# Kernel optimization log

Measured on AMD Instinct MI355X. Metric: run time of the kernel, lower is better.

## Reference

```python
import jax, jax.numpy as jnp
import numpy as np
from jax import lax

B, D, C, K = 8192, 512, 1000, 8
EPS = 1e-8
TEMP = 0.2
NEG = -10000.0


def setup_inputs() -> dict:
    key = jax.random.key(0)
    ks = jax.random.split(key, 6)
    z = jax.random.normal(ks[0], (B, D), dtype=jnp.float32)
    n_exp = jax.random.randint(ks[1], (B,), 0, K, dtype=jnp.int32)
    s1 = 1.0 / np.sqrt(D)
    W1 = jax.random.normal(ks[2], (K, D, D), dtype=jnp.float32) * s1
    b1 = jax.random.normal(ks[3], (K, D), dtype=jnp.float32) * 0.01
    W2 = jax.random.normal(ks[4], (K, D, C), dtype=jnp.float32) * s1
    b2 = jax.random.normal(ks[5], (K, C), dtype=jnp.float32) * 0.01
    return {"z": z, "n_exp": n_exp, "W1": W1, "b1": b1, "W2": W2, "b2": b2}


def _gates_one(p, c, n):
    # p: [K,C] softmax probs for one sample; c: [K] confidences; n: scalar int
    pn = p / (jnp.linalg.norm(p, axis=-1, keepdims=True) + EPS)
    S = pn @ pn.T  # [K,K] pairwise cosine similarity
    sel0 = jnp.zeros((K,), dtype=bool).at[jnp.argmax(c)].set(True)

    def body(t, sel):
        # max cosine sim of each candidate to already-selected set
        max_sim = jnp.max(jnp.where(sel[None, :], S, -jnp.inf), axis=1)
        dist = jnp.where(sel, -jnp.inf, 1.0 - max_sim)
        new = sel.at[jnp.argmax(dist)].set(True)
        return jnp.where(t < n, new, sel)

    sel = lax.fori_loop(1, K, body, sel0)
    gate_logits = jnp.where(sel, c, NEG) / TEMP
    return jax.nn.softmax(gate_logits)


def reference(z, n_exp, W1, b1, W2, b2):
    # K expert MLPs, batched: [B,d] -> [B,K,C]
    h = jax.nn.relu(jnp.einsum('bd,kde->bke', z, W1) + b1[None])
    logits_all = jnp.einsum('bke,kec->bkc', h, W2) + b2[None]
    probs = jax.nn.softmax(logits_all, axis=-1)
    conf = jnp.max(probs, axis=-1)  # [B,K]
    gates = jax.vmap(_gates_one)(probs, conf, n_exp)  # [B,K]
    logits = jnp.einsum('bkc,bk->bc', logits_all, gates)
    return logits, gates
```

## Files before the change

kernel.cpp:

```cpp
#include <hip/hip_runtime.h>
#include <math.h>

#define B_SZ 8192
#define D_DIM 512
#define C_DIM 1000
#define C_PAD 1024
#define K_EXP 8
#define TEMP_INV 5.0f
#define EPS_N 1e-8f

typedef __attribute__((ext_vector_type(8))) short frag_ab;
typedef __attribute__((ext_vector_type(4))) float frag_cd;

__device__ __forceinline__ short f2bf(float f) {
    unsigned u = __builtin_bit_cast(unsigned, f);
    unsigned r = (u + 0x7fffu + ((u >> 16) & 1u)) >> 16;
    return (short)r;
}
__device__ __forceinline__ float bf2f(short s) {
    unsigned u = ((unsigned)(unsigned short)s) << 16;
    return __builtin_bit_cast(float, u);
}
__device__ __forceinline__ void split2(float v, short& s0, short& s1) {
    s0 = f2bf(v);
    s1 = f2bf(v - bf2f(s0));
}

__device__ __forceinline__ void gl_lds16(const short* g, short* l) {
    __builtin_amdgcn_global_load_lds(
        (const __attribute__((address_space(1))) unsigned int*)(const void*)g,
        (__attribute__((address_space(3))) unsigned int*)(void*)l,
        16, 0, 0);
}

__global__ __launch_bounds__(256) void prep_z(const float* __restrict__ z,
                                              short* __restrict__ p0, short* __restrict__ p1) {
    int idx = blockIdx.x * 256 + threadIdx.x;
    float v = z[idx];
    short a, b; split2(v, a, b);
    p0[idx] = a; p1[idx] = b;
}

__global__ __launch_bounds__(256) void prep_w1t(const float* __restrict__ W1,
                                                short* __restrict__ p0, short* __restrict__ p1) {
    __shared__ float t[32][33];
    const int k = blockIdx.z;
    const int d0 = blockIdx.x * 32;
    const int e0 = blockIdx.y * 32;
    const int tx = threadIdx.x & 31, ty = threadIdx.x >> 5;
    const float* src = W1 + ((size_t)k << 18);
#pragma unroll
    for (int r = 0; r < 4; r++) {
        int d = d0 + ty + 8 * r;
        t[ty + 8 * r][tx] = src[(size_t)d * 512 + e0 + tx];
    }
    __syncthreads();
#pragma unroll
    for (int r = 0; r < 4; r++) {
        int e = e0 + ty + 8 * r;
        int d = d0 + tx;
        float v = t[tx][ty + 8 * r];
        short a, b; split2(v, a, b);
        size_t o = ((size_t)k << 18) + (size_t)e * 512 + d;
        p0[o] = a; p1[o] = b;
    }
}

__global__ __launch_bounds__(256) void prep_w2t(const float* __restrict__ W2,
                                                short* __restrict__ p0, short* __restrict__ p1) {
    __shared__ float t[32][33];
    const int k = blockIdx.z;
    const int e0 = blockIdx.x * 32;
    const int c0 = blockIdx.y * 32;
    const int tx = threadIdx.x & 31, ty = threadIdx.x >> 5;
    const float* src = W2 + (size_t)k * (D_DIM * C_DIM);
#pragma unroll
    for (int r = 0; r < 4; r++) {
        int e = e0 + ty + 8 * r;
        int c = c0 + tx;
        t[ty + 8 * r][tx] = (c < C_DIM) ? src[(size_t)e * C_DIM + c] : 0.f;
    }
    __syncthreads();
#pragma unroll
    for (int r = 0; r < 4; r++) {
        int c = c0 + ty + 8 * r;
        int e = e0 + tx;
        float v = t[tx][ty + 8 * r];
        short a, b; split2(v, a, b);
        size_t o = (size_t)k * (C_PAD * D_DIM) + (size_t)c * 512 + e;
        p0[o] = a; p1[o] = b;
    }
}

__global__ __launch_bounds__(256, 2) void gemm_split(
    const short* __restrict__ A0, const short* __restrict__ A1, long long aBatch,
    const short* __restrict__ B0, const short* __restrict__ B1, long long bBatch,
    const float* __restrict__ bias, int biasBatch,
    float* __restrict__ Cf, long long cBatch, int ldc, int Nout,
    short* __restrict__ H0, short* __restrict__ H1, long long hBatch,
    int mt, int nt, int mode)
{
    const int lin = blockIdx.x;
    const int k = lin & 7;
    const int rem = lin >> 3;
    const int gm = (mt >= 4) ? 4 : mt;
    const int win = rem / (gm * nt);
    const int local = rem % (gm * nt);
    const int m0 = (win * gm + local / nt) * 128;
    const int n0 = (local % nt) * 128;

    const int tid = threadIdx.x;
    const int lane = tid & 63;
    const int wv = tid >> 6;
    const int wm = (wv & 1) * 64;
    const int wn = (wv >> 1) * 64;

    __shared__ short lds[32768];

    const short* gA0 = A0 + (size_t)k * aBatch + (size_t)m0 * 512;
    const short* gA1 = A1 + (size_t)k * aBatch + (size_t)m0 * 512;
    const short* gB0 = B0 + (size_t)k * bBatch + (size_t)n0 * 512;
    const short* gB1 = B1 + (size_t)k * bBatch + (size_t)n0 * 512;

    frag_cd acc[4][4];
#pragma unroll
    for (int i = 0; i < 4; i++)
#pragma unroll
        for (int j = 0; j < 4; j++)
            acc[i][j] = (frag_cd){0.f, 0.f, 0.f, 0.f};

    const int srow = tid >> 2;
    const int sch  = (tid & 3) * 8;

    auto stage = [&](int k0, short* buf) {
        short* bA = buf;
        short* bB = buf + 8192;
        const short* ga[2] = {gA0, gA1};
        const short* gb[2] = {gB0, gB1};
#pragma unroll
        for (int p = 0; p < 2; p++)
#pragma unroll
            for (int hh = 0; hh < 2; hh++) {
                int row = hh * 64 + srow;
                gl_lds16(ga[p] + (size_t)row * 512 + k0 + sch, bA + p * 4096 + row * 32 + sch);
                gl_lds16(gb[p] + (size_t)row * 512 + k0 + sch, bB + p * 4096 + row * 32 + sch);
            }
    };

    stage(0, lds);

    for (int it = 0; it < 16; it++) {
        short* curb = lds + (it & 1) * 16384;
        short* nxtb = lds + ((it + 1) & 1) * 16384;
        __syncthreads();
        if (it + 1 < 16) stage((it + 1) * 32, nxtb);

        short* ldsA = curb;
        short* ldsB = curb + 8192;
        frag_ab af[2][4], bfr[2][4];
#pragma unroll
        for (int p = 0; p < 2; p++)
#pragma unroll
            for (int t = 0; t < 4; t++) {
                af[p][t]  = *(const frag_ab*)(ldsA + p * 4096 + (wm + t * 16 + (lane & 15)) * 32 + (lane >> 4) * 8);
                bfr[p][t] = *(const frag_ab*)(ldsB + p * 4096 + (wn + t * 16 + (lane & 15)) * 32 + (lane >> 4) * 8);
            }

#pragma unroll
        for (int i = 0; i < 4; i++)
#pragma unroll
            for (int j = 0; j < 4; j++) {
                frag_cd c = acc[i][j];
                c = __builtin_amdgcn_mfma_f32_16x16x32_bf16(af[0][i], bfr[0][j], c, 0, 0, 0);
                c = __builtin_amdgcn_mfma_f32_16x16x32_bf16(af[0][i], bfr[1][j], c, 0, 0, 0);
                c = __builtin_amdgcn_mfma_f32_16x16x32_bf16(af[1][i], bfr[0][j], c, 0, 0, 0);
                acc[i][j] = c;
            }
    }

    const int r0 = (lane >> 4) * 4;
    const int cc = lane & 15;
    if (mode == 0) {
        float* C = Cf + (size_t)k * cBatch;
        const float* bb = bias + (size_t)k * biasBatch;
#pragma unroll
        for (int i = 0; i < 4; i++) {
            int rowb = m0 + wm + i * 16 + r0;
#pragma unroll
            for (int j = 0; j < 4; j++) {
                int col = n0 + wn + j * 16 + cc;
                if (col < Nout) {
                    float b = bb[col];
#pragma unroll
                    for (int r = 0; r < 4; r++)
                        C[(size_t)(rowb + r) * ldc + col] = acc[i][j][r] + b;
                }
            }
        }
    } else {
        short* h0 = H0 + (size_t)k * hBatch;
        short* h1 = H1 + (size_t)k * hBatch;
        const float* bb = bias + (size_t)k * biasBatch;
#pragma unroll
        for (int i = 0; i < 4; i++) {
            int rowb = m0 + wm + i * 16 + r0;
#pragma unroll
            for (int j = 0; j < 4; j++) {
                int col = n0 + wn + j * 16 + cc;
                float b = bb[col];
#pragma unroll
                for (int r = 0; r < 4; r++) {
                    float v = fmaxf(acc[i][j][r] + b, 0.f);
                    short s0, s1; split2(v, s0, s1);
                    size_t o = (size_t)(rowb + r) * 512 + col;
                    h0[o] = s0; h1[o] = s1;
                }
            }
        }
    }
}

__global__ __launch_bounds__(256) void gate_combine(
    const float* __restrict__ L,
    const int* __restrict__ n_exp,
    float* __restrict__ out_logits,
    float* __restrict__ out_gates,
    int Bc)
{
    const int wv = threadIdx.x >> 6;
    const int lane = threadIdx.x & 63;
    const int b = blockIdx.x * 4 + wv;
    const size_t kcs = (size_t)Bc * C_DIM;
    const float* Lb = L + (size_t)b * C_DIM;

    __shared__ float Sm[4][64];
    __shared__ float Zm[4][8];

    float mx[K_EXP], Zs[K_EXP], dd[36];
#pragma unroll
    for (int k = 0; k < K_EXP; k++) { mx[k] = -INFINITY; Zs[k] = 0.f; }
#pragma unroll
    for (int p = 0; p < 36; p++) dd[p] = 0.f;

    for (int c = lane; c < C_DIM; c += 64) {
        float e[K_EXP];
#pragma unroll
        for (int k = 0; k < K_EXP; k++) {
            float l = Lb[(size_t)k * kcs + c];
            mx[k] = fmaxf(mx[k], l);
            e[k] = __expf(l);
            Zs[k] += e[k];
        }
        int idx = 0;
#pragma unroll
        for (int i = 0; i < K_EXP; i++)
#pragma unroll
            for (int j = i; j < K_EXP; j++) {
                dd[idx] = fmaf(e[i], e[j], dd[idx]);
                idx++;
            }
    }

#pragma unroll
    for (int off = 32; off > 0; off >>= 1) {
#pragma unroll
        for (int k = 0; k < K_EXP; k++) {
            mx[k] = fmaxf(mx[k], __shfl_xor(mx[k], off, 64));
            Zs[k] += __shfl_xor(Zs[k], off, 64);
        }
#pragma unroll
        for (int p = 0; p < 36; p++)
            dd[p] += __shfl_xor(dd[p], off, 64);
    }

    if (lane == 0) {
        int idx = 0;
#pragma unroll
        for (int i = 0; i < K_EXP; i++)
#pragma unroll
            for (int j = i; j < K_EXP; j++) {
                Sm[wv][i * 8 + j] = dd[idx];
                Sm[wv][j * 8 + i] = dd[idx];
                idx++;
            }
#pragma unroll
        for (int k = 0; k < K_EXP; k++) Zm[wv][k] = Zs[k];
    }

    const int ti = lane >> 3, tj = lane & 7;
    const float Zi = Zm[wv][ti], Zj = Zm[wv][tj];
    const float dij = Sm[wv][ti * 8 + tj];
    const float dii = Sm[wv][ti * 8 + ti];
    const float djj = Sm[wv][tj * 8 + tj];
    const float ni = sqrtf(dii) / Zi + EPS_N;
    const float nj = sqrtf(djj) / Zj + EPS_N;
    const float cosij = (dij / (Zi * Zj)) / (ni * nj);

    float conf[K_EXP];
#pragma unroll
    for (int k = 0; k < K_EXP; k++) conf[k] = __expf(mx[k]) / Zs[k];

    int i0 = 0; float bcf = conf[0];
#pragma unroll
    for (int k = 1; k < K_EXP; k++)
        if (conf[k] > bcf) { bcf = conf[k]; i0 = k; }
    unsigned sel = 1u << i0;
    const int n = n_exp[b];

    for (int t = 1; t < K_EXP; t++) {
        float v = ((sel >> tj) & 1u) ? cosij : -INFINITY;
        v = fmaxf(v, __shfl_xor(v, 1, 64));
        v = fmaxf(v, __shfl_xor(v, 2, 64));
        v = fmaxf(v, __shfl_xor(v, 4, 64));
        float dist = ((sel >> ti) & 1u) ? -INFINITY : 1.0f - v;
        float bv = dist; int bi = ti;
#pragma unroll
        for (int off = 8; off < 64; off <<= 1) {
            float ov = __shfl_xor(bv, off, 64);
            int oi = __shfl_xor(bi, off, 64);
            if (ov > bv || (ov == bv && oi < bi)) { bv = ov; bi = oi; }
        }
        if (t < n) sel |= 1u << bi;
    }

    float cmax = -INFINITY;
#pragma unroll
    for (int k = 0; k < K_EXP; k++)
        if ((sel >> k) & 1u) cmax = fmaxf(cmax, conf[k]);
    float g[K_EXP], gsum = 0.f;
#pragma unroll
    for (int k = 0; k < K_EXP; k++) {
        g[k] = ((sel >> k) & 1u) ? __expf((conf[k] - cmax) * TEMP_INV) : 0.f;
        gsum += g[k];
    }
    const float ginv = 1.0f / gsum;
#pragma unroll
    for (int k = 0; k < K_EXP; k++) g[k] *= ginv;

    if (lane == 0) {
        float4* og = (float4*)(out_gates + (size_t)b * K_EXP);
        og[0] = make_float4(g[0], g[1], g[2], g[3]);
        og[1] = make_float4(g[4], g[5], g[6], g[7]);
    }

    for (int c = lane; c < C_DIM; c += 64) {
        float o = 0.f;
#pragma unroll
        for (int k = 0; k < K_EXP; k++)
            o = fmaf(g[k], Lb[(size_t)k * kcs + c], o);
        out_logits[(size_t)b * C_DIM + c] = o;
    }
}

extern "C" void kernel_launch(void* const* d_in, const int* in_sizes, int n_in,
                              void* d_out, int out_size, void* d_ws, size_t ws_size,
                              hipStream_t stream) {
    const float* z     = (const float*)d_in[0];
    const int*   n_exp = (const int*)d_in[1];
    const float* W1    = (const float*)d_in[2];
    const float* b1    = (const float*)d_in[3];
    const float* W2    = (const float*)d_in[4];
    const float* b2    = (const float*)d_in[5];
    float* out_logits = (float*)d_out;
    float* out_gates  = (float*)d_out + (size_t)B_SZ * C_DIM;

    const size_t zP   = (size_t)B_SZ * D_DIM * 2;
    const size_t w1P  = (size_t)K_EXP * D_DIM * D_DIM * 2;
    const size_t w2P  = (size_t)K_EXP * C_PAD * D_DIM * 2;
    const size_t fixedBytes = 2 * (zP + w1P + w2P);

    int nch = 1;
    while (nch < 32 && fixedBytes + (size_t)(B_SZ / nch) * 48384 > ws_size) nch *= 2;
    const int Bc = B_SZ / nch;

    char* w = (char*)d_ws;
    short* zp[2];  zp[0]  = (short*)w; zp[1]  = (short*)(w + zP);  w += 2 * zP;
    short* w1t[2]; w1t[0] = (short*)w; w1t[1] = (short*)(w + w1P); w += 2 * w1P;
    short* w2t[2]; w2t[0] = (short*)w; w2t[1] = (short*)(w + w2P); w += 2 * w2P;
    const size_t hP = (size_t)K_EXP * Bc * D_DIM * 2;
    short* hp[2];  hp[0]  = (short*)w; hp[1]  = (short*)(w + hP);  w += 2 * hP;
    float* Lb = (float*)w;

    prep_z <<<dim3((B_SZ * D_DIM) / 256), 256, 0, stream>>>(z, zp[0], zp[1]);
    prep_w1t<<<dim3(16, 16, K_EXP), 256, 0, stream>>>(W1, w1t[0], w1t[1]);
    prep_w2t<<<dim3(16, 32, K_EXP), 256, 0, stream>>>(W2, w2t[0], w2t[1]);

    const int mt = Bc / 128;

    for (int ch = 0; ch < nch; ch++) {
        const int off = ch * Bc;
        const long long zoff = (long long)off * D_DIM;

        gemm_split<<<dim3(8 * mt * 4), 256, 0, stream>>>(
            zp[0] + zoff, zp[1] + zoff, 0LL,
            w1t[0], w1t[1], (long long)D_DIM * D_DIM,
            b1, D_DIM,
            nullptr, 0LL, 0, D_DIM,
            hp[0], hp[1], (long long)Bc * D_DIM,
            mt, 4, 1);

        gemm_split<<<dim3(8 * mt * 8), 256, 0, stream>>>(
            hp[0], hp[1], (long long)Bc * D_DIM,
            w2t[0], w2t[1], (long long)C_PAD * D_DIM,
            b2, C_DIM,
            Lb, (long long)Bc * C_DIM, C_DIM, C_DIM,
            nullptr, nullptr, 0LL,
            mt, 8, 0);

        gate_combine<<<dim3(Bc / 4), 256, 0, stream>>>(
            Lb, n_exp + off,
            out_logits + (size_t)off * C_DIM,
            out_gates + (size_t)off * K_EXP,
            Bc);
    }
}
```

Baseline: 516.6 us.

## Enlarge GEMM tile to 256x128, add XOR-swizzled LDS, drop double buffering

```diff
diff --git a/kernel.cpp b/kernel.cpp
--- a/kernel.cpp
+++ b/kernel.cpp
@@ -103,79 +103,88 @@
     const int lin = blockIdx.x;
     const int k = lin & 7;
     const int rem = lin >> 3;
-    const int gm = (mt >= 4) ? 4 : mt;
+    const int gm = (mt >= 2) ? 2 : 1;
     const int win = rem / (gm * nt);
     const int local = rem % (gm * nt);
-    const int m0 = (win * gm + local / nt) * 128;
+    const int m0 = (win * gm + local / nt) * 256;
     const int n0 = (local % nt) * 128;
 
     const int tid = threadIdx.x;
     const int lane = tid & 63;
     const int wv = tid >> 6;
-    const int wm = (wv & 1) * 64;
+    const int wm = (wv & 1) * 128;
     const int wn = (wv >> 1) * 64;
 
-    __shared__ short lds[32768];
+    __shared__ short lds[24576];
 
     const short* gA0 = A0 + (size_t)k * aBatch + (size_t)m0 * 512;
     const short* gA1 = A1 + (size_t)k * aBatch + (size_t)m0 * 512;
     const short* gB0 = B0 + (size_t)k * bBatch + (size_t)n0 * 512;
     const short* gB1 = B1 + (size_t)k * bBatch + (size_t)n0 * 512;
-
-    frag_cd acc[4][4];
-#pragma unroll
-    for (int i = 0; i < 4; i++)
+    short* ldsA = lds;
+    short* ldsB = lds + 16384;
+
+    frag_cd acc[8][4];
+#pragma unroll
+    for (int i = 0; i < 8; i++)
 #pragma unroll
         for (int j = 0; j < 4; j++)
             acc[i][j] = (frag_cd){0.f, 0.f, 0.f, 0.f};
 
     const int srow = tid >> 2;
-    const int sch  = (tid & 3) * 8;
-
-    auto stage = [&](int k0, short* buf) {
-        short* bA = buf;
-        short* bB = buf + 8192;
+    const int sc   = tid & 3;
+
+    for (int k0 = 0; k0 < 512; k0 += 32) {
         const short* ga[2] = {gA0, gA1};
         const short* gb[2] = {gB0, gB1};
 #pragma unroll
-        for (int p = 0; p < 2; p++)
+        for (int p = 0; p < 2; p++) {
+#pragma unroll
+            for (int hh = 0; hh < 4; hh++) {
+                int row = hh * 64 + srow;
+                int gq = sc ^ ((row >> 1) & 3);
+                gl_lds16(ga[p] + (size_t)row * 512 + k0 + gq * 8,
+                         ldsA + p * 8192 + row * 32 + sc * 8);
+            }
 #pragma unroll
             for (int hh = 0; hh < 2; hh++) {
                 int row = hh * 64 + srow;
-                gl_lds16(ga[p] + (size_t)row * 512 + k0 + sch, bA + p * 4096 + row * 32 + sch);
-                gl_lds16(gb[p] + (size_t)row * 512 + k0 + sch, bB + p * 4096 + row * 32 + sch);
-            }
-    };
-
-    stage(0, lds);
-
-    for (int it = 0; it < 16; it++) {
-        short* curb = lds + (it & 1) * 16384;
-        short* nxtb = lds + ((it + 1) & 1) * 16384;
+                int gq = sc ^ ((row >> 1) & 3);
+                gl_lds16(gb[p] + (size_t)row * 512 + k0 + gq * 8,
+                         ldsB + p * 4096 + row * 32 + sc * 8);
+            }
+        }
         __syncthreads();
-        if (it + 1 < 16) stage((it + 1) * 32, nxtb);
-
-        short* ldsA = curb;
-        short* ldsB = curb + 8192;
-        frag_ab af[2][4], bfr[2][4];
+
+        const int q = lane >> 4;
+        const int rb = lane & 15;
+
+        frag_ab bfr[2][4];
 #pragma unroll
         for (int p = 0; p < 2; p++)
 #pragma unroll
-            for (int t = 0; t < 4; t++) {
-                af[p][t]  = *(const frag_ab*)(ldsA + p * 4096 + (wm + t * 16 + (lane & 15)) * 32 + (lane >> 4) * 8);
-                bfr[p][t] = *(const frag_ab*)(ldsB + p * 4096 + (wn + t * 16 + (lane & 15)) * 32 + (lane >> 4) * 8);
-            }
-
-#pragma unroll
-        for (int i = 0; i < 4; i++)
+            for (int j = 0; j < 4; j++) {
+                int R = wn + j * 16 + rb;
+                int slot = q ^ ((R >> 1) & 3);
+                bfr[p][j] = *(const frag_ab*)(ldsB + p * 4096 + R * 32 + slot * 8);
+            }
+
+#pragma unroll
+        for (int i = 0; i < 8; i++) {
+            int R = wm + i * 16 + rb;
+            int slot = q ^ ((R >> 1) & 3);
+            frag_ab a0 = *(const frag_ab*)(ldsA + R * 32 + slot * 8);
+            frag_ab a1 = *(const frag_ab*)(ldsA + 8192 + R * 32 + slot * 8);
 #pragma unroll
             for (int j = 0; j < 4; j++) {
                 frag_cd c = acc[i][j];
-                c = __builtin_amdgcn_mfma_f32_16x16x32_bf16(af[0][i], bfr[0][j], c, 0, 0, 0);
-                c = __builtin_amdgcn_mfma_f32_16x16x32_bf16(af[0][i], bfr[1][j], c, 0, 0, 0);
-                c = __builtin_amdgcn_mfma_f32_16x16x32_bf16(af[1][i], bfr[0][j], c, 0, 0, 0);
+                c = __builtin_amdgcn_mfma_f32_16x16x32_bf16(a0, bfr[0][j], c, 0, 0, 0);
+                c = __builtin_amdgcn_mfma_f32_16x16x32_bf16(a0, bfr[1][j], c, 0, 0, 0);
+                c = __builtin_amdgcn_mfma_f32_16x16x32_bf16(a1, bfr[0][j], c, 0, 0, 0);
                 acc[i][j] = c;
             }
+        }
+        __syncthreads();
     }
 
     const int r0 = (lane >> 4) * 4;
@@ -184,7 +193,7 @@
         float* C = Cf + (size_t)k * cBatch;
         const float* bb = bias + (size_t)k * biasBatch;
 #pragma unroll
-        for (int i = 0; i < 4; i++) {
+        for (int i = 0; i < 8; i++) {
             int rowb = m0 + wm + i * 16 + r0;
 #pragma unroll
             for (int j = 0; j < 4; j++) {
@@ -202,7 +211,7 @@
         short* h1 = H1 + (size_t)k * hBatch;
         const float* bb = bias + (size_t)k * biasBatch;
 #pragma unroll
-        for (int i = 0; i < 4; i++) {
+        for (int i = 0; i < 8; i++) {
             int rowb = m0 + wm + i * 16 + r0;
 #pragma unroll
             for (int j = 0; j < 4; j++) {
@@ -385,7 +394,7 @@
     prep_w1t<<<dim3(16, 16, K_EXP), 256, 0, stream>>>(W1, w1t[0], w1t[1]);
     prep_w2t<<<dim3(16, 32, K_EXP), 256, 0, stream>>>(W2, w2t[0], w2t[1]);
 
-    const int mt = Bc / 128;
+    const int mt = Bc / 256;
 
     for (int ch = 0; ch < nch; ch++) {
         const int off = ch * Bc;
```

Result: faster. 479.2 us (-7.2%).
